# Optimization experiments

Measured on AMD Instinct MI355X. Metric: run time of the kernel, lower is better.

## Reference

```python
import jax, jax.numpy as jnp
import numpy as np

N_NODES = 100000
N_EDGES = 1600000
IN_DIM, HID_DIM, OUT_DIM = 128, 256, 1


def setup_inputs() -> dict:
    key = jax.random.key(0)
    ks = jax.random.split(key, 8)
    x = jax.random.normal(ks[0], (N_NODES, IN_DIM), dtype=jnp.float32)
    edge_index = jax.random.randint(ks[1], (2, N_EDGES), 0, N_NODES, dtype=jnp.int64)
    # Glorot-ish scaled params (values arbitrary; shapes match GCNConv/Linear)
    W1 = jax.random.normal(ks[2], (IN_DIM, HID_DIM), dtype=jnp.float32) / np.sqrt(IN_DIM)
    b1 = jnp.zeros((HID_DIM,), dtype=jnp.float32)
    W2 = jax.random.normal(ks[3], (HID_DIM, HID_DIM), dtype=jnp.float32) / np.sqrt(HID_DIM)
    b2 = jnp.zeros((HID_DIM,), dtype=jnp.float32)
    Wout = jax.random.normal(ks[4], (HID_DIM, OUT_DIM), dtype=jnp.float32) / np.sqrt(HID_DIM)
    bout = jnp.zeros((OUT_DIM,), dtype=jnp.float32)
    return {"x": x, "edge_index": edge_index, "W1": W1, "b1": b1,
            "W2": W2, "b2": b2, "Wout": Wout, "bout": bout}


def _gcn_norm(edge_index, num_nodes):
    # add self loops, compute symmetric normalization deg^-1/2[src]*deg^-1/2[dst]
    loops = jnp.arange(num_nodes, dtype=edge_index.dtype)
    src = jnp.concatenate([edge_index[0], loops])
    dst = jnp.concatenate([edge_index[1], loops])
    deg = jax.ops.segment_sum(jnp.ones_like(dst, dtype=jnp.float32), dst,
                              num_segments=num_nodes)
    dinv = jnp.where(deg > 0, jax.lax.rsqrt(deg), 0.0)
    norm = dinv[src] * dinv[dst]  # [E + N]
    return src, dst, norm


def _gcn_layer(x, src, dst, norm, W, b, num_nodes):
    h = x @ W                                   # [N, F_out] dense transform
    msg = h[src] * norm[:, None]                # gather + scale  [E', F_out]
    agg = jax.ops.segment_sum(msg, dst, num_segments=num_nodes)  # scatter-add
    return agg + b


def reference(x, edge_index, W1, b1, W2, b2, Wout, bout):
    n = x.shape[0]
    src, dst, norm = _gcn_norm(edge_index, n)
    h = jax.nn.relu(_gcn_layer(x, src, dst, norm, W1, b1, n))
    h = jax.nn.relu(_gcn_layer(h, src, dst, norm, W2, b2, n))
    pooled = jnp.mean(h, axis=0, keepdims=True)  # global_mean_pool, one graph -> [1, H]
    return pooled @ Wout + bout                  # [1, 1]
```

## Files before the change

kernel.cpp:

```cpp
#include <hip/hip_runtime.h>
#include <hip/hip_bf16.h>


typedef __attribute__((ext_vector_type(8))) short short8;
typedef __attribute__((ext_vector_type(4))) float f32x4;
typedef __attribute__((ext_vector_type(2))) float f32x2;

#define BKT_SHIFT 8
#define BKT_NODES 256
#define BIN_CHUNK 8192
#define CAP 4608
#define PSLOTS 64

__device__ inline unsigned short f2bf(float f) {
    union { float f; unsigned u; } v; v.f = f;
    unsigned r = (v.u + 0x7fff + ((v.u >> 16) & 1)) >> 16;
    return (unsigned short)r;
}

__global__ __launch_bounds__(256) void prep_k(const int* __restrict__ ei,
                                              int* __restrict__ bcur,
                                              uint2* __restrict__ pairs,
                                              const float* __restrict__ x,
                                              unsigned* __restrict__ Xs,
                                              const float* __restrict__ W1,
                                              unsigned short* __restrict__ Wt1,
                                              const float* __restrict__ W2,
                                              unsigned short* __restrict__ Wt2,
                                              int E, int N, int NB,
                                              int NCHUNK, int NCVT) {
    int b = blockIdx.x;
    int tid = threadIdx.x;
    if (b < NCHUNK) {
        __shared__ int hist[512];
        __shared__ int base[512];
        int chunk0 = b * BIN_CHUNK;
        for (int t = tid; t < NB; t += 256) hist[t] = 0;
        __syncthreads();
#pragma unroll 4
        for (int i = 0; i < BIN_CHUNK / 256; ++i) {
            int e = chunk0 + i * 256 + tid;
            if (e < E) {
                unsigned d = (unsigned)ei[(size_t)E + e];
                if (d < (unsigned)N) atomicAdd(&hist[d >> BKT_SHIFT], 1);
            }
        }
        __syncthreads();
        for (int t = tid; t < NB; t += 256) {
            int c = hist[t];
            base[t] = c ? (t * CAP + atomicAdd(&bcur[t], c)) : 0;
            hist[t] = 0;
        }
        __syncthreads();
#pragma unroll 4
        for (int i = 0; i < BIN_CHUNK / 256; ++i) {
            int e = chunk0 + i * 256 + tid;
            if (e < E) {
                unsigned d = (unsigned)ei[(size_t)E + e];
                unsigned s = (unsigned)ei[e];
                if (d < (unsigned)N) {
                    int bb = d >> BKT_SHIFT;
                    int r = atomicAdd(&hist[bb], 1);
                    unsigned sc = (s < (unsigned)N) ? s : 0u;
                    pairs[base[bb] + r] = make_uint2(sc, d);
                }
            }
        }
    } else if (b < NCHUNK + NCVT) {
        int idx = (b - NCHUNK) * 256 + tid;
        if (idx < N * 32) {
            float4 v = ((const float4*)x)[idx];
            float a = fminf(fmaxf(v.x, -448.f), 448.f);
            float bb = fminf(fmaxf(v.y, -448.f), 448.f);
            float c = fminf(fmaxf(v.z, -448.f), 448.f);
            float d = fminf(fmaxf(v.w, -448.f), 448.f);
            int p = __builtin_amdgcn_cvt_pk_fp8_f32(a, bb, 0, false);
            p = __builtin_amdgcn_cvt_pk_fp8_f32(c, d, p, true);
            Xs[idx] = (unsigned)p;
        }
    } else if (b < NCHUNK + NCVT + 128) {
        int idx = (b - NCHUNK - NCVT) * 256 + tid;
        int k = idx >> 8, nn = idx & 255;
        Wt1[nn * 128 + k] = f2bf(W1[idx]);
    } else {
        int idx = (b - NCHUNK - NCVT - 128) * 256 + tid;
        int k = idx >> 8, nn = idx & 255;
        Wt2[nn * 256 + k] = f2bf(W2[idx]);
    }
}

__global__ __launch_bounds__(512) void scatter_k(const uint2* __restrict__ pairs,
                                                 const int* __restrict__ bcur,
                                                 int* __restrict__ off,
                                                 int* __restrict__ deg,
                                                 float* __restrict__ dinv,
                                                 int* __restrict__ csr, int N) {
    __shared__ int h[2][256];
    __shared__ int cur[256];
    int b = blockIdx.x, t = threadIdx.x;
    int lo = b << BKT_SHIFT;
    int rs = b * CAP;
    int re = rs + min(bcur[b], CAP);
    if (t < 256) h[0][t] = 0;
    __syncthreads();
    for (int i = rs + t; i < re; i += 512)
        atomicAdd(&h[0][pairs[i].y - lo], 1);
    __syncthreads();
    int v = (t < 256) ? h[0][t] : 0;
    int cu = 0;
    for (int o = 1; o < 256; o <<= 1) {
        int val = 0;
        if (t < 256) { val = h[cu][t]; if (t >= o) val += h[cu][t - o]; }
        __syncthreads();
        if (t < 256) h[cu ^ 1][t] = val;
        cu ^= 1;
        __syncthreads();
    }
    if (t < 256) {
        int no = rs + (h[cu][t] - v);
        if (lo + t < N) {
            off[lo + t] = no;
            deg[lo + t] = v;
            dinv[lo + t] = rsqrtf((float)v + 1.0f);
        }
        cur[t] = no;
    }
    __syncthreads();
    for (int i = rs + t; i < re; i += 512) {
        uint2 p = pairs[i];
        int pos = atomicAdd(&cur[p.y - lo], 1);
        csr[pos] = (int)p.x;
    }
}

__global__ __launch_bounds__(256) void agg128_k(const unsigned short* __restrict__ X8,
                                                const int* __restrict__ csr,
                                                const int* __restrict__ off,
                                                const int* __restrict__ deg,
                                                const float* __restrict__ dinv,
                                                unsigned short* __restrict__ O8, int n) {
    int w = (blockIdx.x * 256 + threadIdx.x) >> 6;
    int lane = threadIdx.x & 63;
    if (w >= n) return;
    int st = off[w], c = deg[w];
    float di = dinv[w];
    f32x2 sv = __builtin_amdgcn_cvt_pk_f32_fp8((int)X8[(size_t)w * 64 + lane], false);
    float ax[4], ay[4];
    ax[0] = di * sv[0]; ay[0] = di * sv[1];
    ax[1] = ax[2] = ax[3] = 0.f; ay[1] = ay[2] = ay[3] = 0.f;
    int e = 0;
    for (; e + 8 <= c; e += 8) {
        int s[8];
#pragma unroll
        for (int j = 0; j < 8; ++j) s[j] = csr[st + e + j];
        float wd[8];
#pragma unroll
        for (int j = 0; j < 8; ++j) wd[j] = dinv[s[j]];
        unsigned short u[8];
#pragma unroll
        for (int j = 0; j < 8; ++j) u[j] = X8[(size_t)s[j] * 64 + lane];
#pragma unroll
        for (int j = 0; j < 8; ++j) {
            f32x2 f = __builtin_amdgcn_cvt_pk_f32_fp8((int)u[j], false);
            ax[j & 3] += wd[j] * f[0]; ay[j & 3] += wd[j] * f[1];
        }
    }
    if (e + 4 <= c) {
        int s[4];
#pragma unroll
        for (int j = 0; j < 4; ++j) s[j] = csr[st + e + j];
        float wd[4];
#pragma unroll
        for (int j = 0; j < 4; ++j) wd[j] = dinv[s[j]];
        unsigned short u[4];
#pragma unroll
        for (int j = 0; j < 4; ++j) u[j] = X8[(size_t)s[j] * 64 + lane];
#pragma unroll
        for (int j = 0; j < 4; ++j) {
            f32x2 f = __builtin_amdgcn_cvt_pk_f32_fp8((int)u[j], false);
            ax[j] += wd[j] * f[0]; ay[j] += wd[j] * f[1];
        }
        e += 4;
    }
    for (; e < c; ++e) {
        int s = csr[st + e];
        float wd = dinv[s];
        f32x2 f = __builtin_amdgcn_cvt_pk_f32_fp8((int)X8[(size_t)s * 64 + lane], false);
        ax[0] += wd * f[0]; ay[0] += wd * f[1];
    }
    float ox = di * ((ax[0] + ax[1]) + (ax[2] + ax[3]));
    float oy = di * ((ay[0] + ay[1]) + (ay[2] + ay[3]));
    ox = fminf(fmaxf(ox, -448.f), 448.f);
    oy = fminf(fmaxf(oy, -448.f), 448.f);
    int pk = __builtin_amdgcn_cvt_pk_fp8_f32(ox, oy, 0, false);
    O8[(size_t)w * 64 + lane] = (unsigned short)(pk & 0xffff);
}

__global__ __launch_bounds__(256) void agg256_k(const unsigned* __restrict__ H8,
                                                const int* __restrict__ csr,
                                                const int* __restrict__ off,
                                                const int* __restrict__ deg,
                                                const float* __restrict__ dinv,
                                                unsigned* __restrict__ O8, int n) {
    int w = (blockIdx.x * 256 + threadIdx.x) >> 6;
    int lane = threadIdx.x & 63;
    if (w >= n) return;
    int st = off[w], c = deg[w];
    float di = dinv[w];
    unsigned su = H8[(size_t)w * 64 + lane];
    f32x2 slo = __builtin_amdgcn_cvt_pk_f32_fp8((int)su, false);
    f32x2 shi = __builtin_amdgcn_cvt_pk_f32_fp8((int)su, true);
    float a[4][4];
    a[0][0] = slo[0]; a[0][1] = slo[1]; a[0][2] = shi[0]; a[0][3] = shi[1];
#pragma unroll
    for (int g = 1; g < 4; ++g) { a[g][0] = a[g][1] = a[g][2] = a[g][3] = 0.f; }
    int e = 0;
    for (; e + 8 <= c; e += 8) {
        int s[8];
#pragma unroll
        for (int j = 0; j < 8; ++j) s[j] = csr[st + e + j];
        unsigned u[8];
#pragma unroll
        for (int j = 0; j < 8; ++j) u[j] = H8[(size_t)s[j] * 64 + lane];
#pragma unroll
        for (int j = 0; j < 8; ++j) {
            f32x2 lo = __builtin_amdgcn_cvt_pk_f32_fp8((int)u[j], false);
            f32x2 hi = __builtin_amdgcn_cvt_pk_f32_fp8((int)u[j], true);
            a[j & 3][0] += lo[0]; a[j & 3][1] += lo[1];
            a[j & 3][2] += hi[0]; a[j & 3][3] += hi[1];
        }
    }
    if (e + 4 <= c) {
        int s[4];
#pragma unroll
        for (int j = 0; j < 4; ++j) s[j] = csr[st + e + j];
        unsigned u[4];
#pragma unroll
        for (int j = 0; j < 4; ++j) u[j] = H8[(size_t)s[j] * 64 + lane];
#pragma unroll
        for (int j = 0; j < 4; ++j) {
            f32x2 lo = __builtin_amdgcn_cvt_pk_f32_fp8((int)u[j], false);
            f32x2 hi = __builtin_amdgcn_cvt_pk_f32_fp8((int)u[j], true);
            a[j][0] += lo[0]; a[j][1] += lo[1]; a[j][2] += hi[0]; a[j][3] += hi[1];
        }
        e += 4;
    }
    for (; e < c; ++e) {
        int s = csr[st + e];
        unsigned u = H8[(size_t)s * 64 + lane];
        f32x2 lo = __builtin_amdgcn_cvt_pk_f32_fp8((int)u, false);
        f32x2 hi = __builtin_amdgcn_cvt_pk_f32_fp8((int)u, true);
        a[0][0] += lo[0]; a[0][1] += lo[1]; a[0][2] += hi[0]; a[0][3] += hi[1];
    }
    float o0 = di * ((a[0][0] + a[1][0]) + (a[2][0] + a[3][0]));
    float o1 = di * ((a[0][1] + a[1][1]) + (a[2][1] + a[3][1]));
    float o2 = di * ((a[0][2] + a[1][2]) + (a[2][2] + a[3][2]));
    float o3 = di * ((a[0][3] + a[1][3]) + (a[2][3] + a[3][3]));
    o0 = fminf(fmaxf(o0, -448.f), 448.f);
    o1 = fminf(fmaxf(o1, -448.f), 448.f);
    o2 = fminf(fmaxf(o2, -448.f), 448.f);
    o3 = fminf(fmaxf(o3, -448.f), 448.f);
    int pk = __builtin_amdgcn_cvt_pk_fp8_f32(o0, o1, 0, false);
    pk = __builtin_amdgcn_cvt_pk_fp8_f32(o2, o3, pk, true);
    O8[(size_t)w * 64 + lane] = (unsigned)pk;
}

template <int MODE>
__global__ __launch_bounds__(256) void mgemm_k(const unsigned char* __restrict__ A8,
                                               const unsigned short* __restrict__ Bt,
                                               const float* __restrict__ bias,
                                               const float* __restrict__ dinv,
                                               unsigned char* __restrict__ Hout8,
                                               float* __restrict__ pool,
                                               int M, int K) {
    __shared__ __align__(16) char smem[(64 + 256) * 40 * 2];
    short* As = (short*)smem;
    short* Bs = (short*)(smem + 64 * 40 * 2);
    int tid = threadIdx.x;
    int w = tid >> 6, lane = tid & 63, lr = lane >> 4, lc = lane & 15;
    int row0 = blockIdx.x * 64;
    int arow = tid >> 2, akoff = (tid & 3) * 8;
    f32x4 acc[16] = {};

    for (int kt = 0; kt < K; kt += 32) {
        short8 va = {};
        int gr = row0 + arow;
        if (gr < M) {
            uint2 v = *(const uint2*)(A8 + (size_t)gr * K + kt + akoff);
            f32x2 f0 = __builtin_amdgcn_cvt_pk_f32_fp8((int)v.x, false);
            f32x2 f1 = __builtin_amdgcn_cvt_pk_f32_fp8((int)v.x, true);
            f32x2 f2 = __builtin_amdgcn_cvt_pk_f32_fp8((int)v.y, false);
            f32x2 f3 = __builtin_amdgcn_cvt_pk_f32_fp8((int)v.y, true);
            va[0] = (short)f2bf(f0[0]); va[1] = (short)f2bf(f0[1]);
            va[2] = (short)f2bf(f1[0]); va[3] = (short)f2bf(f1[1]);
            va[4] = (short)f2bf(f2[0]); va[5] = (short)f2bf(f2[1]);
            va[6] = (short)f2bf(f3[0]); va[7] = (short)f2bf(f3[1]);
        }
        *(short8*)&As[arow * 40 + akoff] = va;
#pragma unroll
        for (int l = 0; l < 4; ++l) {
            int f = tid + l * 256;
            int br = f >> 2, bk = (f & 3) * 8;
            short8 vb = *(const short8*)(Bt + (size_t)br * K + kt + bk);
            *(short8*)&Bs[br * 40 + bk] = vb;
        }
        __syncthreads();
        short8 af = *(const short8*)&As[(w * 16 + lc) * 40 + lr * 8];
#pragma unroll
        for (int f = 0; f < 16; ++f) {
            short8 bf = *(const short8*)&Bs[(f * 16 + lc) * 40 + lr * 8];
            acc[f] = __builtin_amdgcn_mfma_f32_16x16x32_bf16(af, bf, acc[f], 0, 0, 0);
        }
        __syncthreads();
    }

    float bv[16];
#pragma unroll
    for (int f = 0; f < 16; ++f) bv[f] = bias[f * 16 + lc];

    if (MODE == 1) {
#pragma unroll
        for (int r = 0; r < 4; ++r) {
            int gr = row0 + w * 16 + lr * 4 + r;
            if (gr < M) {
                float dr = dinv[gr];
#pragma unroll
                for (int f = 0; f < 16; ++f) {
                    float v = fminf(dr * fmaxf(acc[f][r] + bv[f], 0.f), 448.f);
                    int p = __builtin_amdgcn_cvt_pk_fp8_f32(v, v, 0, false);
                    Hout8[(size_t)gr * 256 + f * 16 + lc] = (unsigned char)(p & 0xff);
                }
            }
        }
    } else {
        float (*red)[256] = (float(*)[256])smem;
        float s[16];
#pragma unroll
        for (int f = 0; f < 16; ++f) s[f] = 0.f;
#pragma unroll
        for (int r = 0; r < 4; ++r) {
            int gr = row0 + w * 16 + lr * 4 + r;
            if (gr < M) {
#pragma unroll
                for (int f = 0; f < 16; ++f)
                    s[f] += fmaxf(acc[f][r] + bv[f], 0.f);
            }
        }
#pragma unroll
        for (int f = 0; f < 16; ++f) red[w * 4 + lr][f * 16 + lc] = s[f];
        __syncthreads();
        float t = 0.f;
#pragma unroll
        for (int rr = 0; rr < 16; ++rr) t += red[rr][tid];
        atomicAdd(&pool[(blockIdx.x & (PSLOTS - 1)) * 256 + tid], t);
    }
}

__global__ void final_k(const float* __restrict__ pool, const float* __restrict__ Wout,
                        const float* __restrict__ bout, float* __restrict__ out, float invM) {
    __shared__ float s[256];
    int t = threadIdx.x;
    float acc = 0.f;
    for (int sl = 0; sl < PSLOTS; ++sl) acc += pool[sl * 256 + t];
    s[t] = acc * invM * Wout[t];
    __syncthreads();
    for (int o = 128; o > 0; o >>= 1) {
        if (t < o) s[t] += s[t + o];
        __syncthreads();
    }
    if (t == 0) out[0] = s[0] + bout[0];
}

extern "C" void kernel_launch(void* const* d_in, const int* in_sizes, int n_in,
                              void* d_out, int out_size, void* d_ws, size_t ws_size,
                              hipStream_t stream) {
    const float* x    = (const float*)d_in[0];
    const int*   ei   = (const int*)d_in[1];
    const float* W1   = (const float*)d_in[2];
    const float* b1   = (const float*)d_in[3];
    const float* W2   = (const float*)d_in[4];
    const float* b2   = (const float*)d_in[5];
    const float* Wout = (const float*)d_in[6];
    const float* bout = (const float*)d_in[7];
    float* out = (float*)d_out;

    const int N = in_sizes[0] / 128;
    const int E = in_sizes[1] / 2;
    const int NB = (N + BKT_NODES - 1) / BKT_NODES;
    const int NCHUNK = (E + BIN_CHUNK - 1) / BIN_CHUNK;
    const int NCVT = (N * 32 + 255) / 256;

    char* p = (char*)d_ws;
    auto carve = [&](size_t bytes) -> void* {
        void* r = (void*)p;
        p += (bytes + 511) & ~(size_t)511;
        return r;
    };
    unsigned*       Xs   = (unsigned*)carve((size_t)N * 128);
    unsigned short* Xp   = (unsigned short*)carve((size_t)N * 128);
    unsigned char*  H1   = (unsigned char*)carve((size_t)N * 256);
    unsigned*       G    = (unsigned*)carve((size_t)N * 256);
    unsigned short* Wt1  = (unsigned short*)carve((size_t)128 * 256 * 2);
    unsigned short* Wt2  = (unsigned short*)carve((size_t)256 * 256 * 2);
    float* dinv   = (float*)carve((size_t)N * 4);
    int*   off    = (int*)carve((size_t)N * 4);
    int*   deg    = (int*)carve((size_t)N * 4);
    int*   csr    = (int*)carve((size_t)NB * CAP * 4);
    uint2* pairs  = (uint2*)carve((size_t)NB * CAP * 8);
    int*   bcur   = (int*)carve((size_t)NB * 4);
    float* pool   = (float*)carve((size_t)PSLOTS * 256 * 4);

    hipMemsetAsync(bcur, 0, (size_t)NB * 4, stream);
    hipMemsetAsync(pool, 0, (size_t)PSLOTS * 256 * 4, stream);

    prep_k<<<NCHUNK + NCVT + 128 + 256, 256, 0, stream>>>(
        ei, bcur, pairs, x, Xs, W1, Wt1, W2, Wt2, E, N, NB, NCHUNK, NCVT);
    scatter_k<<<NB, 512, 0, stream>>>(pairs, bcur, off, deg, dinv, csr, N);

    agg128_k<<<(N + 3) / 4, 256, 0, stream>>>((const unsigned short*)Xs, csr, off, deg, dinv, Xp, N);
    mgemm_k<1><<<(N + 63) / 64, 256, 0, stream>>>(
        (const unsigned char*)Xp, Wt1, b1, dinv, H1, nullptr, N, 128);

    agg256_k<<<(N + 3) / 4, 256, 0, stream>>>((const unsigned*)H1, csr, off, deg, dinv, G, N);
    mgemm_k<2><<<(N + 63) / 64, 256, 0, stream>>>(
        (const unsigned char*)G, Wt2, b2, nullptr, nullptr, pool, N, 256);

    final_k<<<1, 256, 0, stream>>>(pool, Wout, bout, out, 1.0f / N);
}
```

Before: 259.5 us.

## Pack edge pairs into 32 bits, vectorize aggregation accumulators, double GEMM row tile

Edge (src,dst) pairs are packed into one 32-bit word holding the 17-bit source and the 8-bit local destination, which halves the traffic of the pair buffer between the binning and scatter kernels. The aggregation kernels accumulate into packed float2 vectors so the compiler can emit packed FMA/add. The MFMA GEMM now handles 128 rows per block, with each wave computing two 16-row tiles that share the B fragments, which doubles register accumulators and LDS use. The two memsets are merged into one covering the contiguous bcur..pool region.

```diff
diff --git a/kernel.cpp b/kernel.cpp
--- a/kernel.cpp
+++ b/kernel.cpp
@@ -11,6 +11,8 @@
 #define BIN_CHUNK 8192
 #define CAP 4608
 #define PSLOTS 64
+#define SRC_BITS 17
+#define SRC_MASK 0x1FFFFu
 
 __device__ inline unsigned short f2bf(float f) {
     union { float f; unsigned u; } v; v.f = f;
@@ -20,7 +22,7 @@
 
 __global__ __launch_bounds__(256) void prep_k(const int* __restrict__ ei,
                                               int* __restrict__ bcur,
-                                              uint2* __restrict__ pairs,
+                                              unsigned* __restrict__ pairs,
                                               const float* __restrict__ x,
                                               unsigned* __restrict__ Xs,
                                               const float* __restrict__ W1,
@@ -62,7 +64,7 @@
                     int bb = d >> BKT_SHIFT;
                     int r = atomicAdd(&hist[bb], 1);
                     unsigned sc = (s < (unsigned)N) ? s : 0u;
-                    pairs[base[bb] + r] = make_uint2(sc, d);
+                    pairs[base[bb] + r] = ((d & (BKT_NODES - 1)) << SRC_BITS) | sc;
                 }
             }
         }
@@ -89,7 +91,7 @@
     }
 }
 
-__global__ __launch_bounds__(512) void scatter_k(const uint2* __restrict__ pairs,
+__global__ __launch_bounds__(512) void scatter_k(const unsigned* __restrict__ pairs,
                                                  const int* __restrict__ bcur,
                                                  int* __restrict__ off,
                                                  int* __restrict__ deg,
@@ -104,7 +106,7 @@
     if (t < 256) h[0][t] = 0;
     __syncthreads();
     for (int i = rs + t; i < re; i += 512)
-        atomicAdd(&h[0][pairs[i].y - lo], 1);
+        atomicAdd(&h[0][pairs[i] >> SRC_BITS], 1);
     __syncthreads();
     int v = (t < 256) ? h[0][t] : 0;
     int cu = 0;
@@ -127,9 +129,9 @@
     }
     __syncthreads();
     for (int i = rs + t; i < re; i += 512) {
-        uint2 p = pairs[i];
-        int pos = atomicAdd(&cur[p.y - lo], 1);
-        csr[pos] = (int)p.x;
+        unsigned p = pairs[i];
+        int pos = atomicAdd(&cur[p >> SRC_BITS], 1);
+        csr[pos] = (int)(p & SRC_MASK);
     }
 }
 
@@ -145,9 +147,9 @@
     int st = off[w], c = deg[w];
     float di = dinv[w];
     f32x2 sv = __builtin_amdgcn_cvt_pk_f32_fp8((int)X8[(size_t)w * 64 + lane], false);
-    float ax[4], ay[4];
-    ax[0] = di * sv[0]; ay[0] = di * sv[1];
-    ax[1] = ax[2] = ax[3] = 0.f; ay[1] = ay[2] = ay[3] = 0.f;
+    f32x2 acc[4];
+    acc[0] = di * sv;
+    acc[1] = 0.f; acc[2] = 0.f; acc[3] = 0.f;
     int e = 0;
     for (; e + 8 <= c; e += 8) {
         int s[8];
@@ -162,7 +164,7 @@
 #pragma unroll
         for (int j = 0; j < 8; ++j) {
             f32x2 f = __builtin_amdgcn_cvt_pk_f32_fp8((int)u[j], false);
-            ax[j & 3] += wd[j] * f[0]; ay[j & 3] += wd[j] * f[1];
+            acc[j & 3] += wd[j] * f;
         }
     }
     if (e + 4 <= c) {
@@ -178,7 +180,7 @@
 #pragma unroll
         for (int j = 0; j < 4; ++j) {
             f32x2 f = __builtin_amdgcn_cvt_pk_f32_fp8((int)u[j], false);
-            ax[j] += wd[j] * f[0]; ay[j] += wd[j] * f[1];
+            acc[j] += wd[j] * f;
         }
         e += 4;
     }
@@ -186,12 +188,11 @@
         int s = csr[st + e];
         float wd = dinv[s];
         f32x2 f = __builtin_amdgcn_cvt_pk_f32_fp8((int)X8[(size_t)s * 64 + lane], false);
-        ax[0] += wd * f[0]; ay[0] += wd * f[1];
-    }
-    float ox = di * ((ax[0] + ax[1]) + (ax[2] + ax[3]));
-    float oy = di * ((ay[0] + ay[1]) + (ay[2] + ay[3]));
-    ox = fminf(fmaxf(ox, -448.f), 448.f);
-    oy = fminf(fmaxf(oy, -448.f), 448.f);
+        acc[0] += wd * f;
+    }
+    f32x2 tot = (acc[0] + acc[1]) + (acc[2] + acc[3]);
+    float ox = fminf(fmaxf(di * tot[0], -448.f), 448.f);
+    float oy = fminf(fmaxf(di * tot[1], -448.f), 448.f);
     int pk = __builtin_amdgcn_cvt_pk_fp8_f32(ox, oy, 0, false);
     O8[(size_t)w * 64 + lane] = (unsigned short)(pk & 0xffff);
 }
@@ -208,12 +209,11 @@
     int st = off[w], c = deg[w];
     float di = dinv[w];
     unsigned su = H8[(size_t)w * 64 + lane];
-    f32x2 slo = __builtin_amdgcn_cvt_pk_f32_fp8((int)su, false);
-    f32x2 shi = __builtin_amdgcn_cvt_pk_f32_fp8((int)su, true);
-    float a[4][4];
-    a[0][0] = slo[0]; a[0][1] = slo[1]; a[0][2] = shi[0]; a[0][3] = shi[1];
-#pragma unroll
-    for (int g = 1; g < 4; ++g) { a[g][0] = a[g][1] = a[g][2] = a[g][3] = 0.f; }
+    f32x2 al[4], ah[4];
+    al[0] = __builtin_amdgcn_cvt_pk_f32_fp8((int)su, false);
+    ah[0] = __builtin_amdgcn_cvt_pk_f32_fp8((int)su, true);
+    al[1] = 0.f; al[2] = 0.f; al[3] = 0.f;
+    ah[1] = 0.f; ah[2] = 0.f; ah[3] = 0.f;
     int e = 0;
     for (; e + 8 <= c; e += 8) {
         int s[8];
@@ -224,10 +224,8 @@
         for (int j = 0; j < 8; ++j) u[j] = H8[(size_t)s[j] * 64 + lane];
 #pragma unroll
         for (int j = 0; j < 8; ++j) {
-            f32x2 lo = __builtin_amdgcn_cvt_pk_f32_fp8((int)u[j], false);
-            f32x2 hi = __builtin_amdgcn_cvt_pk_f32_fp8((int)u[j], true);
-            a[j & 3][0] += lo[0]; a[j & 3][1] += lo[1];
-            a[j & 3][2] += hi[0]; a[j & 3][3] += hi[1];
+            al[j & 3] += (f32x2)__builtin_amdgcn_cvt_pk_f32_fp8((int)u[j], false);
+            ah[j & 3] += (f32x2)__builtin_amdgcn_cvt_pk_f32_fp8((int)u[j], true);
         }
     }
     if (e + 4 <= c) {
@@ -239,27 +237,23 @@
         for (int j = 0; j < 4; ++j) u[j] = H8[(size_t)s[j] * 64 + lane];
 #pragma unroll
         for (int j = 0; j < 4; ++j) {
-            f32x2 lo = __builtin_amdgcn_cvt_pk_f32_fp8((int)u[j], false);
-            f32x2 hi = __builtin_amdgcn_cvt_pk_f32_fp8((int)u[j], true);
-            a[j][0] += lo[0]; a[j][1] += lo[1]; a[j][2] += hi[0]; a[j][3] += hi[1];
+            al[j] += (f32x2)__builtin_amdgcn_cvt_pk_f32_fp8((int)u[j], false);
+            ah[j] += (f32x2)__builtin_amdgcn_cvt_pk_f32_fp8((int)u[j], true);
         }
         e += 4;
     }
     for (; e < c; ++e) {
         int s = csr[st + e];
         unsigned u = H8[(size_t)s * 64 + lane];
-        f32x2 lo = __builtin_amdgcn_cvt_pk_f32_fp8((int)u, false);
-        f32x2 hi = __builtin_amdgcn_cvt_pk_f32_fp8((int)u, true);
-        a[0][0] += lo[0]; a[0][1] += lo[1]; a[0][2] += hi[0]; a[0][3] += hi[1];
-    }
-    float o0 = di * ((a[0][0] + a[1][0]) + (a[2][0] + a[3][0]));
-    float o1 = di * ((a[0][1] + a[1][1]) + (a[2][1] + a[3][1]));
-    float o2 = di * ((a[0][2] + a[1][2]) + (a[2][2] + a[3][2]));
-    float o3 = di * ((a[0][3] + a[1][3]) + (a[2][3] + a[3][3]));
-    o0 = fminf(fmaxf(o0, -448.f), 448.f);
-    o1 = fminf(fmaxf(o1, -448.f), 448.f);
-    o2 = fminf(fmaxf(o2, -448.f), 448.f);
-    o3 = fminf(fmaxf(o3, -448.f), 448.f);
+        al[0] += (f32x2)__builtin_amdgcn_cvt_pk_f32_fp8((int)u, false);
+        ah[0] += (f32x2)__builtin_amdgcn_cvt_pk_f32_fp8((int)u, true);
+    }
+    f32x2 L = (al[0] + al[1]) + (al[2] + al[3]);
+    f32x2 H = (ah[0] + ah[1]) + (ah[2] + ah[3]);
+    float o0 = fminf(fmaxf(di * L[0], -448.f), 448.f);
+    float o1 = fminf(fmaxf(di * L[1], -448.f), 448.f);
+    float o2 = fminf(fmaxf(di * H[0], -448.f), 448.f);
+    float o3 = fminf(fmaxf(di * H[1], -448.f), 448.f);
     int pk = __builtin_amdgcn_cvt_pk_fp8_f32(o0, o1, 0, false);
     pk = __builtin_amdgcn_cvt_pk_fp8_f32(o2, o3, pk, true);
     O8[(size_t)w * 64 + lane] = (unsigned)pk;
@@ -273,30 +267,40 @@
                                                unsigned char* __restrict__ Hout8,
                                                float* __restrict__ pool,
                                                int M, int K) {
-    __shared__ __align__(16) char smem[(64 + 256) * 40 * 2];
+    __shared__ __align__(16) char smem[(128 + 256) * 40 * 2];
     short* As = (short*)smem;
-    short* Bs = (short*)(smem + 64 * 40 * 2);
+    short* Bs = (short*)(smem + 128 * 40 * 2);
     int tid = threadIdx.x;
     int w = tid >> 6, lane = tid & 63, lr = lane >> 4, lc = lane & 15;
-    int row0 = blockIdx.x * 64;
-    int arow = tid >> 2, akoff = (tid & 3) * 8;
-    f32x4 acc[16] = {};
+    int row0 = blockIdx.x * 128;
+    int arow = tid >> 1, ahalf = (tid & 1) * 16;
+    f32x4 acc0[16] = {};
+    f32x4 acc1[16] = {};
 
     for (int kt = 0; kt < K; kt += 32) {
-        short8 va = {};
+        short8 vlo = {}, vhi = {};
         int gr = row0 + arow;
         if (gr < M) {
-            uint2 v = *(const uint2*)(A8 + (size_t)gr * K + kt + akoff);
+            uint4 v = *(const uint4*)(A8 + (size_t)gr * K + kt + ahalf);
             f32x2 f0 = __builtin_amdgcn_cvt_pk_f32_fp8((int)v.x, false);
             f32x2 f1 = __builtin_amdgcn_cvt_pk_f32_fp8((int)v.x, true);
             f32x2 f2 = __builtin_amdgcn_cvt_pk_f32_fp8((int)v.y, false);
             f32x2 f3 = __builtin_amdgcn_cvt_pk_f32_fp8((int)v.y, true);
-            va[0] = (short)f2bf(f0[0]); va[1] = (short)f2bf(f0[1]);
-            va[2] = (short)f2bf(f1[0]); va[3] = (short)f2bf(f1[1]);
-            va[4] = (short)f2bf(f2[0]); va[5] = (short)f2bf(f2[1]);
-            va[6] = (short)f2bf(f3[0]); va[7] = (short)f2bf(f3[1]);
-        }
-        *(short8*)&As[arow * 40 + akoff] = va;
+            vlo[0] = (short)f2bf(f0[0]); vlo[1] = (short)f2bf(f0[1]);
+            vlo[2] = (short)f2bf(f1[0]); vlo[3] = (short)f2bf(f1[1]);
+            vlo[4] = (short)f2bf(f2[0]); vlo[5] = (short)f2bf(f2[1]);
+            vlo[6] = (short)f2bf(f3[0]); vlo[7] = (short)f2bf(f3[1]);
+            f32x2 g0 = __builtin_amdgcn_cvt_pk_f32_fp8((int)v.z, false);
+            f32x2 g1 = __builtin_amdgcn_cvt_pk_f32_fp8((int)v.z, true);
+            f32x2 g2 = __builtin_amdgcn_cvt_pk_f32_fp8((int)v.w, false);
+            f32x2 g3 = __builtin_amdgcn_cvt_pk_f32_fp8((int)v.w, true);
+            vhi[0] = (short)f2bf(g0[0]); vhi[1] = (short)f2bf(g0[1]);
+            vhi[2] = (short)f2bf(g1[0]); vhi[3] = (short)f2bf(g1[1]);
+            vhi[4] = (short)f2bf(g2[0]); vhi[5] = (short)f2bf(g2[1]);
+            vhi[6] = (short)f2bf(g3[0]); vhi[7] = (short)f2bf(g3[1]);
+        }
+        *(short8*)&As[arow * 40 + ahalf] = vlo;
+        *(short8*)&As[arow * 40 + ahalf + 8] = vhi;
 #pragma unroll
         for (int l = 0; l < 4; ++l) {
             int f = tid + l * 256;
@@ -305,11 +309,13 @@
             *(short8*)&Bs[br * 40 + bk] = vb;
         }
         __syncthreads();
-        short8 af = *(const short8*)&As[(w * 16 + lc) * 40 + lr * 8];
+        short8 af0 = *(const short8*)&As[(w * 32 + lc) * 40 + lr * 8];
+        short8 af1 = *(const short8*)&As[(w * 32 + 16 + lc) * 40 + lr * 8];
 #pragma unroll
         for (int f = 0; f < 16; ++f) {
             short8 bf = *(const short8*)&Bs[(f * 16 + lc) * 40 + lr * 8];
-            acc[f] = __builtin_amdgcn_mfma_f32_16x16x32_bf16(af, bf, acc[f], 0, 0, 0);
+            acc0[f] = __builtin_amdgcn_mfma_f32_16x16x32_bf16(af0, bf, acc0[f], 0, 0, 0);
+            acc1[f] = __builtin_amdgcn_mfma_f32_16x16x32_bf16(af1, bf, acc1[f], 0, 0, 0);
         }
         __syncthreads();
     }
@@ -321,16 +327,26 @@
     if (MODE == 1) {
 #pragma unroll
         for (int r = 0; r < 4; ++r) {
-            int gr = row0 + w * 16 + lr * 4 + r;
+            int gr = row0 + w * 32 + lr * 4 + r;
             if (gr < M) {
                 float dr = dinv[gr];
 #pragma unroll
                 for (int f = 0; f < 16; ++f) {
-                    float v = fminf(dr * fmaxf(acc[f][r] + bv[f], 0.f), 448.f);
+                    float v = fminf(dr * fmaxf(acc0[f][r] + bv[f], 0.f), 448.f);
                     int p = __builtin_amdgcn_cvt_pk_fp8_f32(v, v, 0, false);
                     Hout8[(size_t)gr * 256 + f * 16 + lc] = (unsigned char)(p & 0xff);
                 }
             }
+            int gr1 = gr + 16;
+            if (gr1 < M) {
+                float dr = dinv[gr1];
+#pragma unroll
+                for (int f = 0; f < 16; ++f) {
+                    float v = fminf(dr * fmaxf(acc1[f][r] + bv[f], 0.f), 448.f);
+                    int p = __builtin_amdgcn_cvt_pk_fp8_f32(v, v, 0, false);
+                    Hout8[(size_t)gr1 * 256 + f * 16 + lc] = (unsigned char)(p & 0xff);
+                }
+            }
         }
     } else {
         float (*red)[256] = (float(*)[256])smem;
@@ -339,11 +355,16 @@
         for (int f = 0; f < 16; ++f) s[f] = 0.f;
 #pragma unroll
         for (int r = 0; r < 4; ++r) {
-            int gr = row0 + w * 16 + lr * 4 + r;
+            int gr = row0 + w * 32 + lr * 4 + r;
             if (gr < M) {
 #pragma unroll
                 for (int f = 0; f < 16; ++f)
-                    s[f] += fmaxf(acc[f][r] + bv[f], 0.f);
+                    s[f] += fmaxf(acc0[f][r] + bv[f], 0.f);
+            }
+            if (gr + 16 < M) {
+#pragma unroll
+                for (int f = 0; f < 16; ++f)
+                    s[f] += fmaxf(acc1[f][r] + bv[f], 0.f);
             }
         }
 #pragma unroll
@@ -406,23 +427,22 @@
     int*   off    = (int*)carve((size_t)N * 4);
     int*   deg    = (int*)carve((size_t)N * 4);
     int*   csr    = (int*)carve((size_t)NB * CAP * 4);
-    uint2* pairs  = (uint2*)carve((size_t)NB * CAP * 8);
+    unsigned* pairs = (unsigned*)carve((size_t)NB * CAP * 4);
     int*   bcur   = (int*)carve((size_t)NB * 4);
     float* pool   = (float*)carve((size_t)PSLOTS * 256 * 4);
 
-    hipMemsetAsync(bcur, 0, (size_t)NB * 4, stream);
-    hipMemsetAsync(pool, 0, (size_t)PSLOTS * 256 * 4, stream);
+    hipMemsetAsync(bcur, 0, (size_t)((char*)pool + PSLOTS * 256 * 4 - (char*)bcur), stream);
 
     prep_k<<<NCHUNK + NCVT + 128 + 256, 256, 0, stream>>>(
         ei, bcur, pairs, x, Xs, W1, Wt1, W2, Wt2, E, N, NB, NCHUNK, NCVT);
     scatter_k<<<NB, 512, 0, stream>>>(pairs, bcur, off, deg, dinv, csr, N);
 
     agg128_k<<<(N + 3) / 4, 256, 0, stream>>>((const unsigned short*)Xs, csr, off, deg, dinv, Xp, N);
-    mgemm_k<1><<<(N + 63) / 64, 256, 0, stream>>>(
+    mgemm_k<1><<<(N + 127) / 128, 256, 0, stream>>>(
         (const unsigned char*)Xp, Wt1, b1, dinv, H1, nullptr, N, 128);
 
     agg256_k<<<(N + 3) / 4, 256, 0, stream>>>((const unsigned*)H1, csr, off, deg, dinv, G, N);
-    mgemm_k<2><<<(N + 63) / 64, 256, 0, stream>>>(
+    mgemm_k<2><<<(N + 127) / 128, 256, 0, stream>>>(
         (const unsigned char*)G, Wt2, b2, nullptr, nullptr, pool, N, 256);
 
     final_k<<<1, 256, 0, stream>>>(pool, Wout, bout, out, 1.0f / N);
```

Result: no change. 264.3 us (+1.9%).
